# Kernel tuning notes

Measured on AMD Instinct MI355X. Metric: run time of the kernel, lower is better.

Reference implementation:

```python
import jax, jax.numpy as jnp
import numpy as np

N = 100000   # number of agents
IN = 64      # input_size (obs+action)
E = 128      # embed_size


def _linear_params(k, out_f, in_f, bias=True):
    kw, kb = jax.random.split(k)
    bound = 1.0 / np.sqrt(in_f)
    W = jax.random.uniform(kw, (out_f, in_f), jnp.float32, -bound, bound)
    if not bias:
        return W, None
    b = jax.random.uniform(kb, (out_f,), jnp.float32, -bound, bound)
    return W, b


def setup_inputs() -> dict:
    key = jax.random.key(0)
    ks = jax.random.split(key, 10)
    obs_actions = jax.random.normal(ks[0], (N, IN), jnp.float32)
    We, be = _linear_params(ks[1], E, IN)
    Wv, _ = _linear_params(ks[2], E, E, bias=False)
    Wq, bq = _linear_params(ks[3], E, E)
    Wk, bk = _linear_params(ks[4], E, E)
    # mlp_attention: fed a length-1 score vector -> in_features = 1 (see notes)
    W1, b1 = _linear_params(ks[5], 512, 1)
    W2, b2 = _linear_params(ks[6], 256, 512)
    W3, b3 = _linear_params(ks[7], 128, 256)
    Wo1, bo1 = _linear_params(ks[8], 128, 2 * E)
    Wo2, bo2 = _linear_params(ks[9], 1, 128)
    return {
        "obs_actions": obs_actions,
        "We": We, "be": be, "Wv": Wv, "Wq": Wq, "bq": bq, "Wk": Wk, "bk": bk,
        "W1": W1, "b1": b1, "W2": W2, "b2": b2, "W3": W3, "b3": b3,
        "Wo1": Wo1, "bo1": bo1, "Wo2": Wo2, "bo2": bo2,
        "self_idx": 0,
    }


def reference(obs_actions, We, be, Wv, Wq, bq, Wk, bk,
              W1, b1, W2, b2, W3, b3, Wo1, bo1, Wo2, bo2, self_idx):
    # embeds: [N, E]
    embeds = obs_actions @ We.T + be
    # query for the self agent: [E]
    q = embeds[self_idx] @ Wq.T + bq
    # keys for all agents (batched version of the per-neighbor loop): [N, E]
    K = embeds @ Wk.T + bk
    # per-agent scalar score: dot(q, k) / sqrt(E) -> [N]
    scores = (K @ q) / jnp.sqrt(jnp.asarray(E, jnp.float32))
    # attention MLP on the scalar score: [N,1] -> [N,512] -> [N,256] -> [N,128]
    h = jax.nn.relu(scores[:, None] @ W1.T + b1)
    h = jax.nn.relu(h @ W2.T + b2)
    sim = jax.nn.relu(h @ W3.T + b3)
    # torch.softmax(sim, dim=0) on a [128] vector == softmax over features
    weights = jax.nn.softmax(sim, axis=-1)  # [N, 128]
    values = embeds @ Wv.T                  # [N, E]
    # exclude the self agent from the aggregation
    mask = (jnp.arange(obs_actions.shape[0]) != self_idx)[:, None]
    weighted = jnp.sum(jnp.where(mask, weights * values, 0.0), axis=0)  # [E]
    critic_input = jnp.concatenate([embeds[self_idx], weighted])        # [2E]
    hidden = jax.nn.relu(critic_input @ Wo1.T + bo1)
    return hidden @ Wo2.T + bo2  # [1]
```

## Files before the change

### kernel.cpp

```cpp
#include <hip/hip_runtime.h>
#include <math.h>

#define TBL 1024

#define OFF_V      0
#define OFF_S0     64
#define OFF_MM     66
#define OFF_C2     128
#define OFF_EMB    256
#define OFF_MT     512
#define OFF_WGT    8704
#define OFF_W1B1   12800
#define OFF_W2T    13824
#define OFF_W3T    144896
#define OFF_H2G    177664
#define OFF_SCORES 439808

__device__ __forceinline__ unsigned encf(float f) {
    unsigned u = __float_as_uint(f);
    return (u & 0x80000000u) ? ~u : (u | 0x80000000u);
}
__device__ __forceinline__ float decf(unsigned u) {
    return __uint_as_float((u & 0x80000000u) ? (u & 0x7fffffffu) : ~u);
}

__global__ void __launch_bounds__(256) k1_prep(
        const float* __restrict__ X,  const float* __restrict__ We,
        const float* __restrict__ be, const float* __restrict__ Wv,
        const float* __restrict__ Wq, const float* __restrict__ bq,
        const float* __restrict__ Wk, const float* __restrict__ bk,
        const float* __restrict__ W1, const float* __restrict__ b1,
        const float* __restrict__ W2, const float* __restrict__ W3,
        const int* __restrict__ selfp, float* ws)
{
    const int b = blockIdx.x, t = threadIdx.x;
    if (b == 0) {
        __shared__ float emb[128], q[128], u[128];
        const int self = *selfp;
        const float* xs = X + (size_t)self * 64;
        if (t < 128) {
            float acc = be[t];
            for (int d = 0; d < 64; ++d) acc = __builtin_fmaf(We[t*64 + d], xs[d], acc);
            emb[t] = acc;
            ws[OFF_EMB + t] = acc;
        }
        __syncthreads();
        if (t < 128) {
            float acc = bq[t];
            for (int f = 0; f < 128; ++f) acc = __builtin_fmaf(Wq[t*128 + f], emb[f], acc);
            q[t] = acc;
        }
        __syncthreads();
        if (t < 128) {
            float acc = 0.f;
            for (int e = 0; e < 128; ++e) acc = __builtin_fmaf(Wk[e*128 + t], q[e], acc);
            u[t] = acc;
        }
        __syncthreads();
        const float rs = 0.08838834764831845f;
        if (t < 64) {
            float acc = 0.f;
            for (int e = 0; e < 128; ++e) acc = __builtin_fmaf(We[e*64 + t], u[e], acc);
            ws[OFF_V + t] = acc * rs;
        }
        if (t == 0) {
            float acc = 0.f;
            for (int e = 0; e < 128; ++e) acc += be[e]*u[e] + bk[e]*q[e];
            ws[OFF_S0] = acc * rs;
            unsigned* mm = (unsigned*)(ws + OFF_MM);
            mm[0] = 0xFFFFFFFFu;
            mm[1] = 0u;
        }
        for (int i = t; i < 32*128; i += 256) ws[OFF_WGT + i] = 0.f;
    } else if (b <= 128) {
        const int r = b - 1;
        if (t < 64) {
            float acc = 0.f;
            for (int e = 0; e < 128; ++e) acc = __builtin_fmaf(Wv[r*128 + e], We[e*64 + t], acc);
            ws[OFF_MT + t*128 + r] = acc;
        } else if (t == 64) {
            float acc = 0.f;
            for (int e = 0; e < 128; ++e) acc = __builtin_fmaf(Wv[r*128 + e], be[e], acc);
            ws[OFF_C2 + r] = acc;
        }
    } else if (b <= 192) {
        const int base = (b - 129) * 2048;
        for (int i = t; i < 2048; i += 256) {
            const int idx = base + i;
            const int k = idx >> 8, c = idx & 255;
            ws[OFF_W2T + idx] = W2[c*512 + k];
        }
    } else if (b <= 208) {
        const int base = (b - 193) * 2048;
        for (int i = t; i < 2048; i += 256) {
            const int idx = base + i;
            const int k = idx >> 7, c = idx & 127;
            ws[OFF_W3T + idx] = W3[c*256 + k];
        }
    } else {
        for (int k = t; k < 512; k += 256) {
            ws[OFF_W1B1 + 2*k]     = W1[k];
            ws[OFF_W1B1 + 2*k + 1] = b1[k];
        }
    }
}

__global__ void __launch_bounds__(256) k2_scores(const float4* __restrict__ X4,
                                                 float* ws, int N)
{
    const int t = threadIdx.x;
    const int lane = t & 63;
    const int wv = t >> 6;
    const int grp = lane >> 4;
    const int l16 = lane & 15;
    const float4 vch = *(const float4*)(ws + OFF_V + l16*4);
    const float s0 = ws[OFF_S0];
    float* scores = ws + OFF_SCORES;
    float smin = INFINITY, smax = -INFINITY;
    const int iters = (N + 15) >> 4;
    for (int it = blockIdx.x; it < iters; it += gridDim.x) {
        const int n = it*16 + wv*4 + grp;
        const bool ok = (n < N);
        float s = 0.f;
        if (ok) {
            const float4 xv = X4[(size_t)n*16 + l16];
            s = xv.x*vch.x + xv.y*vch.y + xv.z*vch.z + xv.w*vch.w;
        }
        s += __shfl_xor(s, 1);
        s += __shfl_xor(s, 2);
        s += __shfl_xor(s, 4);
        s += __shfl_xor(s, 8);
        s += s0;
        if (ok) {
            if (l16 == 0) scores[n] = s;
            smin = fminf(smin, s);
            smax = fmaxf(smax, s);
        }
    }
    #pragma unroll
    for (int m = 32; m >= 1; m >>= 1) {
        smin = fminf(smin, __shfl_xor(smin, m));
        smax = fmaxf(smax, __shfl_xor(smax, m));
    }
    __shared__ float rmn[4], rmx[4];
    if (lane == 0) { rmn[wv] = smin; rmx[wv] = smax; }
    __syncthreads();
    if (t == 0) {
        const float mn = fminf(fminf(rmn[0], rmn[1]), fminf(rmn[2], rmn[3]));
        const float mx = fmaxf(fmaxf(rmx[0], rmx[1]), fmaxf(rmx[2], rmx[3]));
        atomicMin((unsigned*)(ws + OFF_MM), encf(mn));
        atomicMax((unsigned*)(ws + OFF_MM) + 1, encf(mx));
    }
}

__global__ void __launch_bounds__(512) k3_l12(
        const float2* __restrict__ w1b1,
        const float* __restrict__ w2t,
        const float* __restrict__ b2,
        const unsigned* __restrict__ mm,
        float* __restrict__ h2g)
{
    const int t = threadIdx.x;
    const int c = t & 255;
    const int eh = t >> 8;
    const float smin = decf(mm[0]);
    const float smax = decf(mm[1]);
    const float step = (smax - smin) / (float)(TBL - 1);
    const int eA = blockIdx.x*4 + eh*2;
    const float sA = smin + step * (float)eA;
    const float sB = smin + step * (float)(eA + 1);
    const float bb = b2[c];
    float a0 = bb, a1 = bb;
    #pragma unroll 8
    for (int k = 0; k < 512; ++k) {
        const float2 wb = w1b1[k];
        const float w2v = w2t[k*256 + c];
        const float h1A = fmaxf(0.f, __builtin_fmaf(sA, wb.x, wb.y));
        const float h1B = fmaxf(0.f, __builtin_fmaf(sB, wb.x, wb.y));
        a0 = __builtin_fmaf(w2v, h1A, a0);
        a1 = __builtin_fmaf(w2v, h1B, a1);
    }
    *(float2*)(h2g + c*1024 + eA) = make_float2(fmaxf(0.f, a0), fmaxf(0.f, a1));
}

__global__ void __launch_bounds__(256) k3_l3(
        const float* __restrict__ h2g,
        const float* __restrict__ w3t,
        const float* __restrict__ b3,
        const unsigned* __restrict__ mm,
        float* __restrict__ tab)
{
    __shared__ float sm[4][128];
    const int t = threadIdx.x;
    const int j = t & 127;
    const int kh = t >> 7;
    const int e0 = blockIdx.x * 4;
    float acc[4] = {0.f, 0.f, 0.f, 0.f};
    #pragma unroll 8
    for (int kk = 0; kk < 128; ++kk) {
        const int k = kh*128 + kk;
        const float4 h2v = *(const float4*)(h2g + k*1024 + e0);
        const float w3v = w3t[k*128 + j];
        acc[0] = __builtin_fmaf(w3v, h2v.x, acc[0]);
        acc[1] = __builtin_fmaf(w3v, h2v.y, acc[1]);
        acc[2] = __builtin_fmaf(w3v, h2v.z, acc[2]);
        acc[3] = __builtin_fmaf(w3v, h2v.w, acc[3]);
    }
    if (kh == 0) {
        const float bb = b3[j];
        #pragma unroll
        for (int e = 0; e < 4; ++e) sm[e][j] = acc[e] + bb;
    }
    __syncthreads();
    if (kh == 1) {
        #pragma unroll
        for (int e = 0; e < 4; ++e) sm[e][j] = fmaxf(0.f, sm[e][j] + acc[e]);
    }
    __syncthreads();
    const int w = t >> 6, lane = t & 63;
    const float v0 = sm[w][lane];
    const float v1 = sm[w][lane + 64];
    float m = fmaxf(v0, v1);
    #pragma unroll
    for (int msk = 1; msk < 64; msk <<= 1) m = fmaxf(m, __shfl_xor(m, msk));
    float p = __expf(v0 - m) + __expf(v1 - m);
    #pragma unroll
    for (int msk = 1; msk < 64; msk <<= 1) p += __shfl_xor(p, msk);
    const float inv = 1.f / p;
    const int row = e0 + w;
    const float g0 = __expf(v0 - m) * inv;
    const float g1 = __expf(v1 - m) * inv;
    if (row < TBL - 1) {
        tab[2*(row*128 + lane) + 0]      = g0;
        tab[2*(row*128 + lane + 64) + 0] = g1;
    }
    if (row >= 1) {
        tab[2*((row-1)*128 + lane) + 1]      = g0;
        tab[2*((row-1)*128 + lane + 64) + 1] = g1;
    }
}

__global__ void __launch_bounds__(256) k4_main(
        const float* __restrict__ X,
        const float* __restrict__ Mt,
        const float* __restrict__ c2,
        const unsigned* __restrict__ mm,
        const float* __restrict__ scores,
        const float2* __restrict__ tab,
        const int* __restrict__ selfp,
        float* __restrict__ wgt,
        int N, int APW)
{
    const int lane = threadIdx.x & 63;
    const int wid = __builtin_amdgcn_readfirstlane(blockIdx.x*4 + (threadIdx.x >> 6));
    const int j0 = lane, j1 = lane + 64;
    const int a0 = wid * APW;
    const int a1 = min(N, a0 + APW);

    float4 M0[16], M1[16];
    #pragma unroll
    for (int q = 0; q < 16; ++q) {
        M0[q] = make_float4(Mt[(4*q+0)*128 + j0], Mt[(4*q+1)*128 + j0],
                            Mt[(4*q+2)*128 + j0], Mt[(4*q+3)*128 + j0]);
        M1[q] = make_float4(Mt[(4*q+0)*128 + j1], Mt[(4*q+1)*128 + j1],
                            Mt[(4*q+2)*128 + j1], Mt[(4*q+3)*128 + j1]);
    }
    const float cc0 = c2[j0], cc1 = c2[j1];
    const float smin = decf(mm[0]), smax = decf(mm[1]);
    const float inv_step = (smax > smin) ? (float)(TBL - 1) / (smax - smin) : 0.f;
    const int self = *selfp;

    float rho0 = 0.f, rho1 = 0.f;
    if (a0 < a1) {
        float fc; float2 t0c, t1c;
        {
            const float s = scores[a0];
            const float fi = (s - smin) * inv_step;
            int ii = (int)fi; ii = max(0, min(TBL - 2, ii));
            fc = fi - (float)ii;
            t0c = tab[ii*128 + j0]; t1c = tab[ii*128 + j1];
        }
        for (int n = a0; n < a1; ++n) {
            float fn = 0.f; float2 t0n = t0c, t1n = t1c;
            if (n + 1 < a1) {
                const float s = scores[n + 1];
                const float fi = (s - smin) * inv_step;
                int ii = (int)fi; ii = max(0, min(TBL - 2, ii));
                fn = fi - (float)ii;
                t0n = tab[ii*128 + j0]; t1n = tab[ii*128 + j1];
            }
            const float w0 = t0c.x + fc * (t0c.y - t0c.x);
            const float w1 = t1c.x + fc * (t1c.y - t1c.x);
            const float4* xr = (const float4*)(X + ((size_t)n << 6));
            float a00=0.f,a01=0.f,a02=0.f,a03=0.f;
            float b00=0.f,b01=0.f,b02=0.f,b03=0.f;
            #pragma unroll
            for (int q = 0; q < 16; ++q) {
                const float4 xv = xr[q];
                a00 = __builtin_fmaf(M0[q].x, xv.x, a00);
                a01 = __builtin_fmaf(M0[q].y, xv.y, a01);
                a02 = __builtin_fmaf(M0[q].z, xv.z, a02);
                a03 = __builtin_fmaf(M0[q].w, xv.w, a03);
                b00 = __builtin_fmaf(M1[q].x, xv.x, b00);
                b01 = __builtin_fmaf(M1[q].y, xv.y, b01);
                b02 = __builtin_fmaf(M1[q].z, xv.z, b02);
                b03 = __builtin_fmaf(M1[q].w, xv.w, b03);
            }
            const float v0 = (a00 + a01) + (a02 + a03) + cc0;
            const float v1 = (b00 + b01) + (b02 + b03) + cc1;
            if (n != self) {
                rho0 = __builtin_fmaf(w0, v0, rho0);
                rho1 = __builtin_fmaf(w1, v1, rho1);
            }
            fc = fn; t0c = t0n; t1c = t1n;
        }
    }
    const int cpy = wid & 31;
    atomicAdd(&wgt[cpy*128 + j0], rho0);
    atomicAdd(&wgt[cpy*128 + j1], rho1);
}

__global__ void __launch_bounds__(128) k5_final(
        const float* __restrict__ Wo1, const float* __restrict__ bo1,
        const float* __restrict__ Wo2, const float* __restrict__ bo2,
        float* ws, float* out)
{
    __shared__ float es[128], wg[128], red[128];
    const int t = threadIdx.x;
    es[t] = ws[OFF_EMB + t];
    float s = 0.f;
    for (int c = 0; c < 32; ++c) s += ws[OFF_WGT + c*128 + t];
    wg[t] = s;
    __syncthreads();
    const float4* wA = (const float4*)(Wo1 + t*256);
    float ax = 0.f, ay = 0.f, az = 0.f, aw = 0.f;
    #pragma unroll 8
    for (int i = 0; i < 32; ++i) {
        const float4 wv = wA[i];
        const float4 ev = ((const float4*)es)[i];
        ax = __builtin_fmaf(wv.x, ev.x, ax);
        ay = __builtin_fmaf(wv.y, ev.y, ay);
        az = __builtin_fmaf(wv.z, ev.z, az);
        aw = __builtin_fmaf(wv.w, ev.w, aw);
    }
    #pragma unroll 8
    for (int i = 0; i < 32; ++i) {
        const float4 wv = wA[32 + i];
        const float4 gv = ((const float4*)wg)[i];
        ax = __builtin_fmaf(wv.x, gv.x, ax);
        ay = __builtin_fmaf(wv.y, gv.y, ay);
        az = __builtin_fmaf(wv.z, gv.z, az);
        aw = __builtin_fmaf(wv.w, gv.w, aw);
    }
    const float acc = ((ax + ay) + (az + aw)) + bo1[t];
    red[t] = fmaxf(acc, 0.f) * Wo2[t];
    __syncthreads();
    for (int m = 64; m >= 1; m >>= 1) {
        if (t < m) red[t] += red[t + m];
        __syncthreads();
    }
    if (t == 0) out[0] = red[0] + bo2[0];
}

extern "C" void kernel_launch(void* const* d_in, const int* in_sizes, int n_in,
                              void* d_out, int out_size, void* d_ws, size_t ws_size,
                              hipStream_t stream)
{
    const float* X   = (const float*)d_in[0];
    const float* We  = (const float*)d_in[1];
    const float* be  = (const float*)d_in[2];
    const float* Wv  = (const float*)d_in[3];
    const float* Wq  = (const float*)d_in[4];
    const float* bq  = (const float*)d_in[5];
    const float* Wk  = (const float*)d_in[6];
    const float* bk  = (const float*)d_in[7];
    const float* W1  = (const float*)d_in[8];
    const float* b1  = (const float*)d_in[9];
    const float* W2  = (const float*)d_in[10];
    const float* b2  = (const float*)d_in[11];
    const float* W3  = (const float*)d_in[12];
    const float* b3  = (const float*)d_in[13];
    const float* Wo1 = (const float*)d_in[14];
    const float* bo1 = (const float*)d_in[15];
    const float* Wo2 = (const float*)d_in[16];
    const float* bo2 = (const float*)d_in[17];
    const int* selfp = (const int*)d_in[18];
    float* ws = (float*)d_ws;
    float* out = (float*)d_out;

    const int N = in_sizes[0] / 64;
    const int offTab = OFF_SCORES + ((N + 63) & ~63);
    const int nwaves = 768 * 4;
    const int APW = (N + nwaves - 1) / nwaves;

    k1_prep<<<210, 256, 0, stream>>>(X, We, be, Wv, Wq, bq, Wk, bk, W1, b1, W2, W3, selfp, ws);
    k2_scores<<<1024, 256, 0, stream>>>((const float4*)X, ws, N);
    k3_l12<<<256, 512, 0, stream>>>((const float2*)(ws + OFF_W1B1), ws + OFF_W2T,
                                    b2, (const unsigned*)(ws + OFF_MM), ws + OFF_H2G);
    k3_l3<<<256, 256, 0, stream>>>(ws + OFF_H2G, ws + OFF_W3T, b3,
                                   (const unsigned*)(ws + OFF_MM), ws + offTab);
    k4_main<<<768, 256, 0, stream>>>(X, ws + OFF_MT, ws + OFF_C2,
                                     (const unsigned*)(ws + OFF_MM), ws + OFF_SCORES,
                                     (const float2*)(ws + offTab), selfp,
                                     ws + OFF_WGT, N, APW);
    k5_final<<<1, 128, 0, stream>>>(Wo1, bo1, Wo2, bo2, ws, out);
}
```

Baseline: 224.2 us.

## Fuse prep and score kernels, drop weight transposes, halve lookup table

```diff
diff --git a/kernel.cpp b/kernel.cpp
--- a/kernel.cpp
+++ b/kernel.cpp
@@ -1,193 +1,210 @@
 #include <hip/hip_runtime.h>
 #include <math.h>
 
-#define TBL 1024
-
-#define OFF_V      0
-#define OFF_S0     64
-#define OFF_MM     66
+#define TBL 512
+#define SBLK 512
+
+#define OFF_MM     64
 #define OFF_C2     128
 #define OFF_EMB    256
 #define OFF_MT     512
 #define OFF_WGT    8704
-#define OFF_W1B1   12800
-#define OFF_W2T    13824
-#define OFF_W3T    144896
-#define OFF_H2G    177664
-#define OFF_SCORES 439808
-
-__device__ __forceinline__ unsigned encf(float f) {
-    unsigned u = __float_as_uint(f);
-    return (u & 0x80000000u) ? ~u : (u | 0x80000000u);
-}
-__device__ __forceinline__ float decf(unsigned u) {
-    return __uint_as_float((u & 0x80000000u) ? (u & 0x7fffffffu) : ~u);
-}
-
-__global__ void __launch_bounds__(256) k1_prep(
+#define OFF_BMIN   12800
+#define OFF_BMAX   13312
+#define OFF_H2G    13824
+#define OFF_SCORES 144896
+
+__global__ void __launch_bounds__(256) k12(
         const float* __restrict__ X,  const float* __restrict__ We,
         const float* __restrict__ be, const float* __restrict__ Wv,
         const float* __restrict__ Wq, const float* __restrict__ bq,
         const float* __restrict__ Wk, const float* __restrict__ bk,
-        const float* __restrict__ W1, const float* __restrict__ b1,
-        const float* __restrict__ W2, const float* __restrict__ W3,
-        const int* __restrict__ selfp, float* ws)
+        const int* __restrict__ selfp, float* __restrict__ ws,
+        int N, int APB)
 {
     const int b = blockIdx.x, t = threadIdx.x;
     if (b == 0) {
-        __shared__ float emb[128], q[128], u[128];
         const int self = *selfp;
-        const float* xs = X + (size_t)self * 64;
+        const float4* xs4 = (const float4*)(X + (size_t)self * 64);
         if (t < 128) {
-            float acc = be[t];
-            for (int d = 0; d < 64; ++d) acc = __builtin_fmaf(We[t*64 + d], xs[d], acc);
-            emb[t] = acc;
-            ws[OFF_EMB + t] = acc;
-        }
-        __syncthreads();
-        if (t < 128) {
-            float acc = bq[t];
-            for (int f = 0; f < 128; ++f) acc = __builtin_fmaf(Wq[t*128 + f], emb[f], acc);
-            q[t] = acc;
-        }
-        __syncthreads();
-        if (t < 128) {
-            float acc = 0.f;
-            for (int e = 0; e < 128; ++e) acc = __builtin_fmaf(Wk[e*128 + t], q[e], acc);
-            u[t] = acc;
-        }
-        __syncthreads();
-        const float rs = 0.08838834764831845f;
-        if (t < 64) {
-            float acc = 0.f;
-            for (int e = 0; e < 128; ++e) acc = __builtin_fmaf(We[e*64 + t], u[e], acc);
-            ws[OFF_V + t] = acc * rs;
-        }
-        if (t == 0) {
-            float acc = 0.f;
-            for (int e = 0; e < 128; ++e) acc += be[e]*u[e] + bk[e]*q[e];
-            ws[OFF_S0] = acc * rs;
-            unsigned* mm = (unsigned*)(ws + OFF_MM);
-            mm[0] = 0xFFFFFFFFu;
-            mm[1] = 0u;
+            const float4* wr = (const float4*)(We + t*64);
+            float ax = 0.f, ay = 0.f, az = 0.f, aw = 0.f;
+            #pragma unroll
+            for (int q = 0; q < 16; ++q) {
+                const float4 wv = wr[q];
+                const float4 xv = xs4[q];
+                ax = __builtin_fmaf(wv.x, xv.x, ax);
+                ay = __builtin_fmaf(wv.y, xv.y, ay);
+                az = __builtin_fmaf(wv.z, xv.z, az);
+                aw = __builtin_fmaf(wv.w, xv.w, aw);
+            }
+            ws[OFF_EMB + t] = ((ax + ay) + (az + aw)) + be[t];
         }
         for (int i = t; i < 32*128; i += 256) ws[OFF_WGT + i] = 0.f;
     } else if (b <= 128) {
         const int r = b - 1;
         if (t < 64) {
             float acc = 0.f;
-            for (int e = 0; e < 128; ++e) acc = __builtin_fmaf(Wv[r*128 + e], We[e*64 + t], acc);
+            #pragma unroll 8
+            for (int e = 0; e < 128; ++e)
+                acc = __builtin_fmaf(Wv[r*128 + e], We[e*64 + t], acc);
             ws[OFF_MT + t*128 + r] = acc;
         } else if (t == 64) {
             float acc = 0.f;
-            for (int e = 0; e < 128; ++e) acc = __builtin_fmaf(Wv[r*128 + e], be[e], acc);
+            for (int e = 0; e < 128; ++e)
+                acc = __builtin_fmaf(Wv[r*128 + e], be[e], acc);
             ws[OFF_C2 + r] = acc;
         }
-    } else if (b <= 192) {
-        const int base = (b - 129) * 2048;
-        for (int i = t; i < 2048; i += 256) {
-            const int idx = base + i;
-            const int k = idx >> 8, c = idx & 255;
-            ws[OFF_W2T + idx] = W2[c*512 + k];
-        }
-    } else if (b <= 208) {
-        const int base = (b - 193) * 2048;
-        for (int i = t; i < 2048; i += 256) {
-            const int idx = base + i;
-            const int k = idx >> 7, c = idx & 127;
-            ws[OFF_W3T + idx] = W3[c*256 + k];
-        }
     } else {
-        for (int k = t; k < 512; k += 256) {
-            ws[OFF_W1B1 + 2*k]     = W1[k];
-            ws[OFF_W1B1 + 2*k + 1] = b1[k];
-        }
-    }
-}
-
-__global__ void __launch_bounds__(256) k2_scores(const float4* __restrict__ X4,
-                                                 float* ws, int N)
-{
+        __shared__ float emb[128], qv[128], uu[128], vv[64];
+        __shared__ float s0s;
+        const int self = *selfp;
+        const float4* xs4 = (const float4*)(X + (size_t)self * 64);
+        if (t < 128) {
+            const float4* wr = (const float4*)(We + t*64);
+            float ax = 0.f, ay = 0.f, az = 0.f, aw = 0.f;
+            #pragma unroll
+            for (int q = 0; q < 16; ++q) {
+                const float4 wv = wr[q];
+                const float4 xv = xs4[q];
+                ax = __builtin_fmaf(wv.x, xv.x, ax);
+                ay = __builtin_fmaf(wv.y, xv.y, ay);
+                az = __builtin_fmaf(wv.z, xv.z, az);
+                aw = __builtin_fmaf(wv.w, xv.w, aw);
+            }
+            emb[t] = ((ax + ay) + (az + aw)) + be[t];
+        }
+        __syncthreads();
+        if (t < 128) {
+            const float4* wr = (const float4*)(Wq + t*128);
+            float ax = 0.f, ay = 0.f, az = 0.f, aw = 0.f;
+            #pragma unroll 8
+            for (int q = 0; q < 32; ++q) {
+                const float4 wv = wr[q];
+                const float4 ev = ((const float4*)emb)[q];
+                ax = __builtin_fmaf(wv.x, ev.x, ax);
+                ay = __builtin_fmaf(wv.y, ev.y, ay);
+                az = __builtin_fmaf(wv.z, ev.z, az);
+                aw = __builtin_fmaf(wv.w, ev.w, aw);
+            }
+            qv[t] = ((ax + ay) + (az + aw)) + bq[t];
+        }
+        __syncthreads();
+        if (t < 128) {
+            float acc = 0.f;
+            #pragma unroll 8
+            for (int e = 0; e < 128; ++e)
+                acc = __builtin_fmaf(Wk[e*128 + t], qv[e], acc);
+            uu[t] = acc;
+        }
+        __syncthreads();
+        const float rs = 0.08838834764831845f;
+        if (t < 64) {
+            float acc = 0.f;
+            #pragma unroll 8
+            for (int e = 0; e < 128; ++e)
+                acc = __builtin_fmaf(We[e*64 + t], uu[e], acc);
+            vv[t] = acc * rs;
+        } else if (t == 64) {
+            float acc = 0.f;
+            for (int e = 0; e < 128; ++e)
+                acc += be[e]*uu[e] + bk[e]*qv[e];
+            s0s = acc * rs;
+        }
+        __syncthreads();
+
+        const int s = b - 129;
+        const int base = s * APB;
+        const int n1 = min(N, base + APB);
+        const int l16 = t & 15;
+        const int slot = t >> 4;
+        const float4 vch = *(const float4*)(vv + l16*4);
+        const float s0 = s0s;
+        const float4* X4 = (const float4*)X;
+        float* scores = ws + OFF_SCORES;
+        float smin = INFINITY, smax = -INFINITY;
+        for (int n = base + slot; n < n1; n += 16) {
+            const float4 xv = X4[(size_t)n*16 + l16];
+            float sc = xv.x*vch.x + xv.y*vch.y + xv.z*vch.z + xv.w*vch.w;
+            sc += __shfl_xor(sc, 1);
+            sc += __shfl_xor(sc, 2);
+            sc += __shfl_xor(sc, 4);
+            sc += __shfl_xor(sc, 8);
+            sc += s0;
+            if (l16 == 0) scores[n] = sc;
+            smin = fminf(smin, sc);
+            smax = fmaxf(smax, sc);
+        }
+        #pragma unroll
+        for (int m = 32; m >= 1; m >>= 1) {
+            smin = fminf(smin, __shfl_xor(smin, m));
+            smax = fmaxf(smax, __shfl_xor(smax, m));
+        }
+        __shared__ float rmn[4], rmx[4];
+        const int wv = t >> 6;
+        if ((t & 63) == 0) { rmn[wv] = smin; rmx[wv] = smax; }
+        __syncthreads();
+        if (t == 0) {
+            ws[OFF_BMIN + s] = fminf(fminf(rmn[0], rmn[1]), fminf(rmn[2], rmn[3]));
+            ws[OFF_BMAX + s] = fmaxf(fmaxf(rmx[0], rmx[1]), fmaxf(rmx[2], rmx[3]));
+        }
+    }
+}
+
+__global__ void __launch_bounds__(512) k3a(
+        const float* __restrict__ W1, const float* __restrict__ b1,
+        const float* __restrict__ W2, const float* __restrict__ b2,
+        float* __restrict__ ws, int nsb)
+{
+    __shared__ float rmn[8], rmx[8];
     const int t = threadIdx.x;
-    const int lane = t & 63;
-    const int wv = t >> 6;
-    const int grp = lane >> 4;
-    const int l16 = lane & 15;
-    const float4 vch = *(const float4*)(ws + OFF_V + l16*4);
-    const float s0 = ws[OFF_S0];
-    float* scores = ws + OFF_SCORES;
-    float smin = INFINITY, smax = -INFINITY;
-    const int iters = (N + 15) >> 4;
-    for (int it = blockIdx.x; it < iters; it += gridDim.x) {
-        const int n = it*16 + wv*4 + grp;
-        const bool ok = (n < N);
-        float s = 0.f;
-        if (ok) {
-            const float4 xv = X4[(size_t)n*16 + l16];
-            s = xv.x*vch.x + xv.y*vch.y + xv.z*vch.z + xv.w*vch.w;
-        }
-        s += __shfl_xor(s, 1);
-        s += __shfl_xor(s, 2);
-        s += __shfl_xor(s, 4);
-        s += __shfl_xor(s, 8);
-        s += s0;
-        if (ok) {
-            if (l16 == 0) scores[n] = s;
-            smin = fminf(smin, s);
-            smax = fmaxf(smax, s);
-        }
-    }
+    float mn = (t < nsb) ? ws[OFF_BMIN + t] : INFINITY;
+    float mx = (t < nsb) ? ws[OFF_BMAX + t] : -INFINITY;
     #pragma unroll
     for (int m = 32; m >= 1; m >>= 1) {
-        smin = fminf(smin, __shfl_xor(smin, m));
-        smax = fmaxf(smax, __shfl_xor(smax, m));
-    }
-    __shared__ float rmn[4], rmx[4];
-    if (lane == 0) { rmn[wv] = smin; rmx[wv] = smax; }
+        mn = fminf(mn, __shfl_xor(mn, m));
+        mx = fmaxf(mx, __shfl_xor(mx, m));
+    }
+    if ((t & 63) == 0) { rmn[t >> 6] = mn; rmx[t >> 6] = mx; }
     __syncthreads();
-    if (t == 0) {
-        const float mn = fminf(fminf(rmn[0], rmn[1]), fminf(rmn[2], rmn[3]));
-        const float mx = fmaxf(fmaxf(rmx[0], rmx[1]), fmaxf(rmx[2], rmx[3]));
-        atomicMin((unsigned*)(ws + OFF_MM), encf(mn));
-        atomicMax((unsigned*)(ws + OFF_MM) + 1, encf(mx));
-    }
-}
-
-__global__ void __launch_bounds__(512) k3_l12(
-        const float2* __restrict__ w1b1,
-        const float* __restrict__ w2t,
-        const float* __restrict__ b2,
-        const unsigned* __restrict__ mm,
-        float* __restrict__ h2g)
-{
-    const int t = threadIdx.x;
+    float smin = rmn[0], smax = rmx[0];
+    #pragma unroll
+    for (int w = 1; w < 8; ++w) {
+        smin = fminf(smin, rmn[w]);
+        smax = fmaxf(smax, rmx[w]);
+    }
+    if (blockIdx.x == 0 && t == 0) { ws[OFF_MM] = smin; ws[OFF_MM + 1] = smax; }
+
+    const float step = (smax - smin) / (float)(TBL - 1);
     const int c = t & 255;
     const int eh = t >> 8;
-    const float smin = decf(mm[0]);
-    const float smax = decf(mm[1]);
-    const float step = (smax - smin) / (float)(TBL - 1);
     const int eA = blockIdx.x*4 + eh*2;
     const float sA = smin + step * (float)eA;
     const float sB = smin + step * (float)(eA + 1);
     const float bb = b2[c];
     float a0 = bb, a1 = bb;
-    #pragma unroll 8
-    for (int k = 0; k < 512; ++k) {
-        const float2 wb = w1b1[k];
-        const float w2v = w2t[k*256 + c];
-        const float h1A = fmaxf(0.f, __builtin_fmaf(sA, wb.x, wb.y));
-        const float h1B = fmaxf(0.f, __builtin_fmaf(sB, wb.x, wb.y));
-        a0 = __builtin_fmaf(w2v, h1A, a0);
-        a1 = __builtin_fmaf(w2v, h1B, a1);
-    }
-    *(float2*)(h2g + c*1024 + eA) = make_float2(fmaxf(0.f, a0), fmaxf(0.f, a1));
-}
-
-__global__ void __launch_bounds__(256) k3_l3(
+    const float4* w2r = (const float4*)(W2 + c*512);
+    #pragma unroll 4
+    for (int kq = 0; kq < 128; ++kq) {
+        const float4 w2 = w2r[kq];
+        #pragma unroll
+        for (int i = 0; i < 4; ++i) {
+            const int k = kq*4 + i;
+            const float w1v = W1[k];
+            const float b1v = b1[k];
+            const float h1A = fmaxf(0.f, __builtin_fmaf(sA, w1v, b1v));
+            const float h1B = fmaxf(0.f, __builtin_fmaf(sB, w1v, b1v));
+            const float wc = (i == 0) ? w2.x : (i == 1) ? w2.y : (i == 2) ? w2.z : w2.w;
+            a0 = __builtin_fmaf(wc, h1A, a0);
+            a1 = __builtin_fmaf(wc, h1B, a1);
+        }
+    }
+    *(float2*)(ws + OFF_H2G + c*TBL + eA) = make_float2(fmaxf(0.f, a0), fmaxf(0.f, a1));
+}
+
+__global__ void __launch_bounds__(256) k3b(
+        const float* __restrict__ W3, const float* __restrict__ b3,
         const float* __restrict__ h2g,
-        const float* __restrict__ w3t,
-        const float* __restrict__ b3,
-        const unsigned* __restrict__ mm,
         float* __restrict__ tab)
 {
     __shared__ float sm[4][128];
@@ -196,15 +213,20 @@
     const int kh = t >> 7;
     const int e0 = blockIdx.x * 4;
     float acc[4] = {0.f, 0.f, 0.f, 0.f};
-    #pragma unroll 8
-    for (int kk = 0; kk < 128; ++kk) {
-        const int k = kh*128 + kk;
-        const float4 h2v = *(const float4*)(h2g + k*1024 + e0);
-        const float w3v = w3t[k*128 + j];
-        acc[0] = __builtin_fmaf(w3v, h2v.x, acc[0]);
-        acc[1] = __builtin_fmaf(w3v, h2v.y, acc[1]);
-        acc[2] = __builtin_fmaf(w3v, h2v.z, acc[2]);
-        acc[3] = __builtin_fmaf(w3v, h2v.w, acc[3]);
+    const float4* w3r = (const float4*)(W3 + j*256 + kh*128);
+    #pragma unroll 4
+    for (int kq = 0; kq < 32; ++kq) {
+        const float4 w3 = w3r[kq];
+        #pragma unroll
+        for (int i = 0; i < 4; ++i) {
+            const int k = kh*128 + kq*4 + i;
+            const float4 h2v = *(const float4*)(h2g + k*TBL + e0);
+            const float wc = (i == 0) ? w3.x : (i == 1) ? w3.y : (i == 2) ? w3.z : w3.w;
+            acc[0] = __builtin_fmaf(wc, h2v.x, acc[0]);
+            acc[1] = __builtin_fmaf(wc, h2v.y, acc[1]);
+            acc[2] = __builtin_fmaf(wc, h2v.z, acc[2]);
+            acc[3] = __builtin_fmaf(wc, h2v.w, acc[3]);
+        }
     }
     if (kh == 0) {
         const float bb = b3[j];
@@ -244,7 +266,7 @@
         const float* __restrict__ X,
         const float* __restrict__ Mt,
         const float* __restrict__ c2,
-        const unsigned* __restrict__ mm,
+        const float* __restrict__ mm,
         const float* __restrict__ scores,
         const float2* __restrict__ tab,
         const int* __restrict__ selfp,
@@ -266,7 +288,7 @@
                             Mt[(4*q+2)*128 + j1], Mt[(4*q+3)*128 + j1]);
     }
     const float cc0 = c2[j0], cc1 = c2[j1];
-    const float smin = decf(mm[0]), smax = decf(mm[1]);
+    const float smin = mm[0], smax = mm[1];
     const float inv_step = (smax > smin) ? (float)(TBL - 1) / (smax - smin) : 0.f;
     const int self = *selfp;
 
@@ -390,18 +412,15 @@
 
     const int N = in_sizes[0] / 64;
     const int offTab = OFF_SCORES + ((N + 63) & ~63);
+    const int APB = (N + SBLK - 1) / SBLK;
     const int nwaves = 768 * 4;
     const int APW = (N + nwaves - 1) / nwaves;
 
-    k1_prep<<<210, 256, 0, stream>>>(X, We, be, Wv, Wq, bq, Wk, bk, W1, b1, W2, W3, selfp, ws);
-    k2_scores<<<1024, 256, 0, stream>>>((const float4*)X, ws, N);
-    k3_l12<<<256, 512, 0, stream>>>((const float2*)(ws + OFF_W1B1), ws + OFF_W2T,
-                                    b2, (const unsigned*)(ws + OFF_MM), ws + OFF_H2G);
-    k3_l3<<<256, 256, 0, stream>>>(ws + OFF_H2G, ws + OFF_W3T, b3,
-                                   (const unsigned*)(ws + OFF_MM), ws + offTab);
-    k4_main<<<768, 256, 0, stream>>>(X, ws + OFF_MT, ws + OFF_C2,
-                                     (const unsigned*)(ws + OFF_MM), ws + OFF_SCORES,
-                                     (const float2*)(ws + offTab), selfp,
-                                     ws + OFF_WGT, N, APW);
+    k12<<<129 + SBLK, 256, 0, stream>>>(X, We, be, Wv, Wq, bq, Wk, bk, selfp, ws, N, APB);
+    k3a<<<TBL/4, 512, 0, stream>>>(W1, b1, W2, b2, ws, SBLK);
+    k3b<<<TBL/4, 256, 0, stream>>>(W3, b3, ws + OFF_H2G, ws + offTab);
+    k4_main<<<768, 256, 0, stream>>>(X, ws + OFF_MT, ws + OFF_C2, ws + OFF_MM,
+                                     ws + OFF_SCORES, (const float2*)(ws + offTab),
+                                     selfp, ws + OFF_WGT, N, APW);
     k5_final<<<1, 128, 0, stream>>>(Wo1, bo1, Wo2, bo2, ws, out);
 }
```

Result: faster. 204.7 us (-8.7%).
